# Kernel tuning notes

Hardware: AMD Instinct MI355X
Metric: run time of the kernel (lower is better)

## Reference

```python
import math
import jax, jax.numpy as jnp
import numpy as np

NH, NKV, HD = 16, 8, 128  # n_heads, n_kv_heads, head_dim from config

def setup_inputs() -> dict:
    key = jax.random.key(0)
    ks = jax.random.split(key, 5)
    B, T, D = 2, 2048, 2048
    KV = NKV * HD  # 1024
    s = 1.0 / math.sqrt(D)
    return {
        "x": jax.random.normal(ks[0], (B, T, D), dtype=jnp.float32),
        "Wq": jax.random.normal(ks[1], (D, D), dtype=jnp.float32) * s,
        "Wk": jax.random.normal(ks[2], (KV, D), dtype=jnp.float32) * s,
        "Wv": jax.random.normal(ks[3], (KV, D), dtype=jnp.float32) * s,
        "Wo": jax.random.normal(ks[4], (D, D), dtype=jnp.float32) * s,
    }

def reference(x, Wq, Wk, Wv, Wo):
    B, T, D = x.shape
    groups = NH // NKV
    scale = 1.0 / math.sqrt(HD)
    # Projections (torch Linear: y = x @ W.T)
    q = (x @ Wq.T).reshape(B, T, NH, HD).transpose(0, 2, 1, 3)    # [B, nh, T, hd]
    k = (x @ Wk.T).reshape(B, T, NKV, HD).transpose(0, 2, 1, 3)   # [B, nkv, T, hd]
    v = (x @ Wv.T).reshape(B, T, NKV, HD).transpose(0, 2, 1, 3)   # [B, nkv, T, hd]
    kv_state = jnp.concatenate([k, v], axis=-1)                    # [B, nkv, T, 2*hd]
    # GQA: replicate kv heads (repeat_interleave along head dim)
    k = jnp.repeat(k, groups, axis=1)                              # [B, nh, T, hd]
    v = jnp.repeat(v, groups, axis=1)
    scores = jnp.einsum('bhqd,bhkd->bhqk', q, k) * scale           # [B, nh, T, T]
    causal = jnp.tril(jnp.ones((T, T), dtype=bool))
    scores = jnp.where(causal, scores, jnp.finfo(scores.dtype).min)
    probs = jax.nn.softmax(scores, axis=-1)
    attn = jnp.einsum('bhqk,bhkd->bhqd', probs, v)                 # [B, nh, T, hd]
    attn = attn.transpose(0, 2, 1, 3).reshape(B, T, NH * HD)
    output = attn @ Wo.T
    return (output, kv_state)
```

## Files before the change

### kernel.cpp

```cpp
#include <hip/hip_runtime.h>
#include <hip/hip_bf16.h>
#include <cstdint>
#include <cstddef>

#define DEV __device__ __forceinline__

typedef __attribute__((ext_vector_type(8))) short short8;
typedef __attribute__((ext_vector_type(4))) float f32x4;
typedef __attribute__((ext_vector_type(8))) __bf16 bf16x8;

DEV unsigned short f2bf(float f) {
    unsigned u = __builtin_bit_cast(unsigned, f);
    u += 0x7fffu + ((u >> 16) & 1u);
    return (unsigned short)(u >> 16);
}

DEV unsigned short f2bf_hw(float f) {
    return __builtin_bit_cast(unsigned short, (__bf16)f);
}

DEV f32x4 mfma16(short8 a, short8 b, f32x4 c) {
    return __builtin_amdgcn_mfma_f32_16x16x32_bf16(
        __builtin_bit_cast(bf16x8, a), __builtin_bit_cast(bf16x8, b), c, 0, 0, 0);
}

#define GLD_TO_LDS16(g, l)                                                  \
    __builtin_amdgcn_global_load_lds(                                       \
        (const __attribute__((address_space(1))) void*)(g),                 \
        (__attribute__((address_space(3))) void*)(l), 16, 0, 0)

__global__ void cvt_all(const float* __restrict__ x,  const float* __restrict__ wq,
                        const float* __restrict__ wk, const float* __restrict__ wv,
                        const float* __restrict__ wo,
                        unsigned short* __restrict__ xb,  unsigned short* __restrict__ wqb,
                        unsigned short* __restrict__ wkb, unsigned short* __restrict__ wvb,
                        unsigned short* __restrict__ wob) {
    constexpr int NX = 1048576, NQ = 524288, NK = 262144, NV = 262144, NO = 524288;
    constexpr int C1 = NX, C2 = C1 + NQ, C3 = C2 + NK, C4 = C3 + NV, C5 = C4 + NO;
    int i = blockIdx.x * blockDim.x + threadIdx.x;
    int stride = gridDim.x * blockDim.x;
    for (; i < C5; i += stride) {
        const float* s;
        unsigned short* d;
        int j;
        if (i < C1)      { s = x;  d = xb;  j = i; }
        else if (i < C2) { s = wq; d = wqb; j = i - C1; }
        else if (i < C3) { s = wk; d = wkb; j = i - C2; }
        else if (i < C4) { s = wv; d = wvb; j = i - C3; }
        else             { s = wo; d = wob; j = i - C4; }
        const f32x4* sp = (const f32x4*)(s + (size_t)j * 8);
        f32x4 a = sp[0], bq = sp[1];
        short8 o;
        o[0] = (short)f2bf(a[0]);  o[1] = (short)f2bf(a[1]);
        o[2] = (short)f2bf(a[2]);  o[3] = (short)f2bf(a[3]);
        o[4] = (short)f2bf(bq[0]); o[5] = (short)f2bf(bq[1]);
        o[6] = (short)f2bf(bq[2]); o[7] = (short)f2bf(bq[3]);
        *(short8*)(d + (size_t)j * 8) = o;
    }
}

__global__ __launch_bounds__(256) void transpose_v(
    const unsigned short* __restrict__ src, unsigned short* __restrict__ dst) {
    __shared__ __align__(16) unsigned short tile[64 * 64];
    const int t0 = blockIdx.x * 64;
    const int d0 = blockIdx.y * 64;
    const int b  = blockIdx.z;
    const int tid = threadIdx.x;
#pragma unroll
    for (int p = 0; p < 2; ++p) {
        int ch = tid + p * 256;
        int it = ch >> 3, ic8 = ch & 7;
        short8 v = *(const short8*)(src + (size_t)(b * 2048 + t0 + it) * 1024 + d0 + ic8 * 8);
        *(short8*)&tile[it * 64 + ((ic8 ^ (it & 7)) << 3)] = v;
    }
    __syncthreads();
#pragma unroll
    for (int p = 0; p < 2; ++p) {
        int ch = tid + p * 256;
        int od = ch >> 3, ot8 = ch & 7;
        short8 v;
#pragma unroll
        for (int j = 0; j < 8; ++j) {
            int t = ot8 * 8 + j;
            v[j] = (short)tile[t * 64 + ((((od >> 3) ^ (t & 7)) << 3) | (od & 7))];
        }
        *(short8*)(dst + (size_t)(b * 1024 + d0 + od) * 2048 + t0 + ot8 * 8) = v;
    }
}

__global__ __launch_bounds__(512, 2) void gemm_qkv_8p(
    const unsigned short* __restrict__ A,
    const unsigned short* __restrict__ Wq, const unsigned short* __restrict__ Wk,
    const unsigned short* __restrict__ Wv,
    unsigned short* __restrict__ Qo, unsigned short* __restrict__ Ko,
    unsigned short* __restrict__ Vo, float* __restrict__ kvf) {
    constexpr int K = 2048, BM = 256, KT = K / 64;
    __shared__ __align__(16) unsigned short sA[2][2][BM][32];
    __shared__ __align__(16) unsigned short sB[2][2][BM][32];

    const int tid = threadIdx.x, lane = tid & 63, w = tid >> 6;
    const int wm = w >> 2, wn = w & 3;
    const int lrow = lane & 15, lg = lane >> 4;
    const int m0 = blockIdx.y * BM, n0 = blockIdx.x * BM;

    const unsigned short* Bp;
    unsigned short* Co;
    int c0, ostr, doff = 0;
    bool iskv = false;
    if (n0 < 2048)      { Bp = Wq + (size_t)n0 * K;        Co = Qo; c0 = n0;        ostr = 2048; }
    else if (n0 < 3072) { Bp = Wk + (size_t)(n0-2048) * K; Co = Ko; c0 = n0 - 2048; ostr = 1024; iskv = true; }
    else                { Bp = Wv + (size_t)(n0-3072) * K; Co = Vo; c0 = n0 - 3072; ostr = 1024; iskv = true; doff = 128; }

    const unsigned short* Ab = A + (size_t)m0 * K;

    auto stage = [&](const unsigned short* gcol, unsigned short* lds) {
#pragma unroll
        for (int p = 0; p < 2; ++p) {
            int ch = tid + p * 512;
            int row = ch >> 2;
            int slot = (ch & 3) ^ (row & 3);
            GLD_TO_LDS16(gcol + (size_t)row * K + slot * 8, lds + ch * 8);
        }
    };

    f32x4 acc[8][4];
#pragma unroll
    for (int i = 0; i < 8; ++i)
#pragma unroll
        for (int j = 0; j < 4; ++j) acc[i][j] = (f32x4)0.f;

    const int xoff = (lg * 8) ^ ((lrow & 3) << 3);
    const int arow0 = wm * 128 + lrow;
    const int brow0 = wn * 64 + lrow;

    stage(Ab,      &sA[0][0][0][0]);
    stage(Bp,      &sB[0][0][0][0]);
    stage(Ab + 32, &sA[0][1][0][0]);
    stage(Bp + 32, &sB[0][1][0][0]);
    asm volatile("s_waitcnt vmcnt(4)\n\ts_barrier" ::: "memory");

    for (int kt = 0; kt < KT; ++kt) {
        const int buf = kt & 1, nb = buf ^ 1;
        const bool pre = (kt + 1 < KT);
        const unsigned short* An = Ab + (kt + 1) * 64;
        const unsigned short* Bn = Bp + (kt + 1) * 64;
        short8 bfrag[4], afrag[4];

        if (pre) stage(An, &sA[nb][0][0][0]);
#pragma unroll
        for (int ni = 0; ni < 4; ++ni)
            bfrag[ni] = *(const short8*)(&sB[buf][0][brow0 + ni * 16][0] + xoff);
#pragma unroll
        for (int mi = 0; mi < 4; ++mi)
            afrag[mi] = *(const short8*)(&sA[buf][0][arow0 + mi * 16][0] + xoff);
        __builtin_amdgcn_s_setprio(1);
#pragma unroll
        for (int mi = 0; mi < 4; ++mi)
#pragma unroll
            for (int ni = 0; ni < 4; ++ni)
                acc[mi][ni] = mfma16(afrag[mi], bfrag[ni], acc[mi][ni]);
        __builtin_amdgcn_s_setprio(0);

        if (pre) stage(Bn, &sB[nb][0][0][0]);
#pragma unroll
        for (int mi = 0; mi < 4; ++mi)
            afrag[mi] = *(const short8*)(&sA[buf][0][arow0 + 64 + mi * 16][0] + xoff);
        __builtin_amdgcn_s_setprio(1);
#pragma unroll
        for (int mi = 0; mi < 4; ++mi)
#pragma unroll
            for (int ni = 0; ni < 4; ++ni)
                acc[4 + mi][ni] = mfma16(afrag[mi], bfrag[ni], acc[4 + mi][ni]);
        __builtin_amdgcn_s_setprio(0);

        if (pre) asm volatile("s_waitcnt vmcnt(4)\n\ts_barrier" ::: "memory");
        else     asm volatile("s_waitcnt vmcnt(0)\n\ts_barrier" ::: "memory");

        if (pre) stage(An + 32, &sA[nb][1][0][0]);
#pragma unroll
        for (int ni = 0; ni < 4; ++ni)
            bfrag[ni] = *(const short8*)(&sB[buf][1][brow0 + ni * 16][0] + xoff);
#pragma unroll
        for (int mi = 0; mi < 4; ++mi)
            afrag[mi] = *(const short8*)(&sA[buf][1][arow0 + mi * 16][0] + xoff);
        __builtin_amdgcn_s_setprio(1);
#pragma unroll
        for (int mi = 0; mi < 4; ++mi)
#pragma unroll
            for (int ni = 0; ni < 4; ++ni)
                acc[mi][ni] = mfma16(afrag[mi], bfrag[ni], acc[mi][ni]);
        __builtin_amdgcn_s_setprio(0);

        if (pre) stage(Bn + 32, &sB[nb][1][0][0]);
#pragma unroll
        for (int mi = 0; mi < 4; ++mi)
            afrag[mi] = *(const short8*)(&sA[buf][1][arow0 + 64 + mi * 16][0] + xoff);
        __builtin_amdgcn_s_setprio(1);
#pragma unroll
        for (int mi = 0; mi < 4; ++mi)
#pragma unroll
            for (int ni = 0; ni < 4; ++ni)
                acc[4 + mi][ni] = mfma16(afrag[mi], bfrag[ni], acc[4 + mi][ni]);
        __builtin_amdgcn_s_setprio(0);

        if (pre) asm volatile("s_waitcnt vmcnt(4)\n\ts_barrier" ::: "memory");
    }

    const int lrow4 = (lane >> 4) * 4, lcol = lane & 15;
#pragma unroll
    for (int mi = 0; mi < 8; ++mi) {
#pragma unroll
        for (int ni = 0; ni < 4; ++ni) {
#pragma unroll
            for (int r = 0; r < 4; ++r) {
                int row = m0 + wm * 128 + mi * 16 + lrow4 + r;
                int col = c0 + wn * 64 + ni * 16 + lcol;
                float v = acc[mi][ni][r];
                Co[(size_t)row * ostr + col] = f2bf(v);
                if (iskv) {
                    int b = row >> 11, t = row & 2047;
                    int kh = col >> 7, d = col & 127;
                    kvf[((size_t)(b * 8 + kh) * 2048 + t) * 256 + doff + d] = v;
                }
            }
        }
    }
}

__global__ __launch_bounds__(512, 2) void gemm_o_2p(
    const unsigned short* __restrict__ A, const unsigned short* __restrict__ Bm,
    float* __restrict__ Cf) {
    constexpr int K = 2048, N = 2048, KT = K / 64;
    __shared__ __align__(16) unsigned short sA[2][2][256][32];
    __shared__ __align__(16) unsigned short sB[2][2][128][32];

    const int tid = threadIdx.x, lane = tid & 63, w = tid >> 6;
    const int wm = w >> 1, wn = w & 1;
    const int lrow = lane & 15, lg = lane >> 4;
    const int m0 = blockIdx.y * 256, n0 = blockIdx.x * 128;

    const unsigned short* Ab = A + (size_t)m0 * K;
    const unsigned short* Bb = Bm + (size_t)n0 * K;

    auto stageA = [&](const unsigned short* gcol, unsigned short* lds) {
#pragma unroll
        for (int p = 0; p < 2; ++p) {
            int ch = tid + p * 512;
            int row = ch >> 2;
            int slot = (ch & 3) ^ (row & 3);
            GLD_TO_LDS16(gcol + (size_t)row * K + slot * 8, lds + ch * 8);
        }
    };
    auto stageB = [&](const unsigned short* gcol, unsigned short* lds) {
        int ch = tid;
        int row = ch >> 2;
        int slot = (ch & 3) ^ (row & 3);
        GLD_TO_LDS16(gcol + (size_t)row * K + slot * 8, lds + ch * 8);
    };

    f32x4 acc[4][4];
#pragma unroll
    for (int i = 0; i < 4; ++i)
#pragma unroll
        for (int j = 0; j < 4; ++j) acc[i][j] = (f32x4)0.f;

    const int xoff = (lg * 8) ^ ((lrow & 3) << 3);
    const int arow0 = wm * 64 + lrow;
    const int brow0 = wn * 64 + lrow;

    stageA(Ab,      &sA[0][0][0][0]);
    stageB(Bb,      &sB[0][0][0][0]);
    stageA(Ab + 32, &sA[0][1][0][0]);
    stageB(Bb + 32, &sB[0][1][0][0]);
    asm volatile("s_waitcnt vmcnt(3)\n\ts_barrier" ::: "memory");

    for (int kt = 0; kt < KT; ++kt) {
        const int buf = kt & 1, nb = buf ^ 1;
        const bool pre = (kt + 1 < KT);
        const unsigned short* An = Ab + (kt + 1) * 64;
        const unsigned short* Bn = Bb + (kt + 1) * 64;
        short8 afrag[4], bfrag[4];

        if (pre) { stageA(An, &sA[nb][0][0][0]); stageB(Bn, &sB[nb][0][0][0]); }
#pragma unroll
        for (int ni = 0; ni < 4; ++ni)
            bfrag[ni] = *(const short8*)(&sB[buf][0][brow0 + ni * 16][0] + xoff);
#pragma unroll
        for (int mi = 0; mi < 4; ++mi)
            afrag[mi] = *(const short8*)(&sA[buf][0][arow0 + mi * 16][0] + xoff);
        __builtin_amdgcn_s_setprio(1);
#pragma unroll
        for (int mi = 0; mi < 4; ++mi)
#pragma unroll
            for (int ni = 0; ni < 4; ++ni)
                acc[mi][ni] = mfma16(afrag[mi], bfrag[ni], acc[mi][ni]);
        __builtin_amdgcn_s_setprio(0);

        if (pre) asm volatile("s_waitcnt vmcnt(3)\n\ts_barrier" ::: "memory");
        else     asm volatile("s_waitcnt vmcnt(0)\n\ts_barrier" ::: "memory");

        if (pre) { stageA(An + 32, &sA[nb][1][0][0]); stageB(Bn + 32, &sB[nb][1][0][0]); }
#pragma unroll
        for (int ni = 0; ni < 4; ++ni)
            bfrag[ni] = *(const short8*)(&sB[buf][1][brow0 + ni * 16][0] + xoff);
#pragma unroll
        for (int mi = 0; mi < 4; ++mi)
            afrag[mi] = *(const short8*)(&sA[buf][1][arow0 + mi * 16][0] + xoff);
        __builtin_amdgcn_s_setprio(1);
#pragma unroll
        for (int mi = 0; mi < 4; ++mi)
#pragma unroll
            for (int ni = 0; ni < 4; ++ni)
                acc[mi][ni] = mfma16(afrag[mi], bfrag[ni], acc[mi][ni]);
        __builtin_amdgcn_s_setprio(0);

        if (pre) asm volatile("s_waitcnt vmcnt(3)\n\ts_barrier" ::: "memory");
    }

    const int lrow4 = (lane >> 4) * 4, lcol = lane & 15;
#pragma unroll
    for (int mi = 0; mi < 4; ++mi)
#pragma unroll
        for (int ni = 0; ni < 4; ++ni)
#pragma unroll
            for (int r = 0; r < 4; ++r) {
                int row = m0 + wm * 64 + mi * 16 + lrow4 + r;
                int col = n0 + wn * 64 + ni * 16 + lcol;
                Cf[(size_t)row * N + col] = acc[mi][ni][r];
            }
}

__global__ __launch_bounds__(512, 2) void attn_fwd(
    const unsigned short* __restrict__ Qb, const unsigned short* __restrict__ Kb,
    const unsigned short* __restrict__ Vtg, unsigned short* __restrict__ Ob) {
    constexpr int T = 2048, DQ = 2048, DKV = 1024, HD = 128;
    constexpr float SC2 = 0.08838834764831845f * 1.4426950408889634f;
    constexpr float SHIFT = 8.0f * 1.4426950408889634f;
    __shared__ __align__(16) unsigned short Ks[2][64][128];
    __shared__ __align__(16) unsigned short Vs[2][128][64];
    __shared__ __align__(16) unsigned short Ps[8][16][64];

    const int bx = blockIdx.x, kh = blockIdx.y, b = blockIdx.z;
    const int qtile = b ? (31 - bx) : bx;
    const int tid = threadIdx.x, lane = tid & 63, w = tid >> 6;
    const int h = kh * 2 + (w >> 2);
    const int lrow = lane & 15, lg = lane >> 4;
    const int qt0 = qtile * 64;
    const int qrow0 = qt0 + (w & 3) * 16;
    const size_t bT = (size_t)b * T;

    short8 qf[4];
    {
        const unsigned short* qbase = Qb + (bT + qrow0 + lrow) * DQ + h * HD + lg * 8;
#pragma unroll
        for (int kc = 0; kc < 4; ++kc) qf[kc] = *(const short8*)(qbase + kc * 32);
    }

    int kr[2], kc8[2], vd[2], vk8[2];
#pragma unroll
    for (int p = 0; p < 2; ++p) {
        int ch = tid + p * 512;
        kr[p] = ch >> 4;  kc8[p] = ch & 15;
        vd[p] = ch >> 3;  vk8[p] = ch & 7;
    }
    const unsigned short* kbase = Kb + bT * DKV + kh * HD;
    const unsigned short* vbase = Vtg + (size_t)(b * 8 + kh) * 128 * T;
    short8 kreg[2], vreg[2];
    auto gload = [&](int kt) {
#pragma unroll
        for (int p = 0; p < 2; ++p) {
            kreg[p] = *(const short8*)(kbase + (size_t)(kt * 64 + kr[p]) * DKV + kc8[p] * 8);
            vreg[p] = *(const short8*)(vbase + (size_t)vd[p] * T + kt * 64 + vk8[p] * 8);
        }
    };
    auto lwrite = [&](int buf) {
#pragma unroll
        for (int p = 0; p < 2; ++p) {
            *(short8*)&Ks[buf][kr[p]][(kc8[p] ^ (kr[p] & 15)) << 3] = kreg[p];
            *(short8*)&Vs[buf][vd[p]][(vk8[p] ^ (vd[p] & 7)) << 3] = vreg[p];
        }
    };

    f32x4 o[8];
#pragma unroll
    for (int i = 0; i < 8; ++i) o[i] = (f32x4)0.f;
    float rsum[4] = {0.f, 0.f, 0.f, 0.f};

    const int nkt = qtile + 1;
    gload(0);
    for (int kt = 0; kt < nkt; ++kt) {
        const int kt0 = kt * 64;
        const int buf = kt & 1;
        lwrite(buf);
        __syncthreads();
        if (kt + 1 < nkt) gload(kt + 1);

        f32x4 s[4];
        __builtin_amdgcn_s_setprio(1);
#pragma unroll
        for (int nt = 0; nt < 4; ++nt) {
            s[nt] = (f32x4)0.f;
#pragma unroll
            for (int kc = 0; kc < 4; ++kc) {
                short8 kf = *(const short8*)&Ks[buf][nt * 16 + lrow][((kc * 4 + lg) ^ lrow) << 3];
                s[nt] = mfma16(qf[kc], kf, s[nt]);
            }
        }
        __builtin_amdgcn_s_setprio(0);

        const int qabs = qrow0 + lg * 4;
        const bool diag = (kt == qtile);
#pragma unroll
        for (int nt = 0; nt < 4; ++nt) {
            int kcol = kt0 + nt * 16 + lrow;
#pragma unroll
            for (int r = 0; r < 4; ++r) {
                float p = exp2f(fmaf(s[nt][r], SC2, -SHIFT));
                if (diag && kcol > qabs + r) p = 0.f;
                rsum[r] += p;
                int q = lg * 4 + r;
                Ps[w][q][((((nt * 2) + (lrow >> 3)) ^ (q & 7)) << 3) | (lrow & 7)] = f2bf_hw(p);
            }
        }

        __builtin_amdgcn_s_setprio(1);
#pragma unroll
        for (int kc2 = 0; kc2 < 2; ++kc2) {
            short8 pf = *(const short8*)&Ps[w][lrow][((kc2 * 4 + lg) ^ (lrow & 7)) << 3];
#pragma unroll
            for (int dt = 0; dt < 8; ++dt) {
                int d = dt * 16 + lrow;
                short8 vf = *(const short8*)&Vs[buf][d][((kc2 * 4 + lg) ^ (d & 7)) << 3];
                o[dt] = mfma16(pf, vf, o[dt]);
            }
        }
        __builtin_amdgcn_s_setprio(0);
    }

#pragma unroll
    for (int r = 0; r < 4; ++r) {
        float v = rsum[r];
        v += __shfl_xor(v, 1);
        v += __shfl_xor(v, 2);
        v += __shfl_xor(v, 4);
        v += __shfl_xor(v, 8);
        float inv = 1.f / v;
        int row = qrow0 + lg * 4 + r;
        unsigned short* obase = Ob + (bT + row) * DQ + h * HD + lrow;
#pragma unroll
        for (int dt = 0; dt < 8; ++dt) obase[dt * 16] = f2bf_hw(o[dt][r] * inv);
    }
}

extern "C" void kernel_launch(void* const* d_in, const int* in_sizes, int n_in,
                              void* d_out, int out_size, void* d_ws, size_t ws_size,
                              hipStream_t stream) {
    (void)in_sizes; (void)n_in; (void)out_size; (void)ws_size;
    const float* x  = (const float*)d_in[0];
    const float* Wq = (const float*)d_in[1];
    const float* Wk = (const float*)d_in[2];
    const float* Wv = (const float*)d_in[3];
    const float* Wo = (const float*)d_in[4];
    float* out = (float*)d_out;
    float* kv_out = out + (size_t)8388608;

    unsigned short* xb   = (unsigned short*)d_ws;
    unsigned short* wqb  = xb   + 8388608;
    unsigned short* wkb  = wqb  + 4194304;
    unsigned short* wvb  = wkb  + 2097152;
    unsigned short* wob  = wvb  + 2097152;
    unsigned short* qb   = wob  + 4194304;
    unsigned short* kb   = qb   + 8388608;
    unsigned short* vt   = kb   + 4194304;
    unsigned short* ab   = vt   + 4194304;
    unsigned short* vtmp = ab;

    cvt_all<<<dim3(2048), dim3(256), 0, stream>>>(x, Wq, Wk, Wv, Wo,
                                                  xb, wqb, wkb, wvb, wob);
    gemm_qkv_8p<<<dim3(16, 16), 512, 0, stream>>>(xb, wqb, wkb, wvb, qb, kb, vtmp, kv_out);
    transpose_v<<<dim3(32, 16, 2), 256, 0, stream>>>(vtmp, vt);
    attn_fwd<<<dim3(32, 8, 2), 512, 0, stream>>>(qb, kb, vt, ab);
    gemm_o_2p<<<dim3(16, 16), 512, 0, stream>>>(ab, wob, out);
}
```

Before: 252.1 us.

## Stream K/V directly to LDS and pass P through register permutes

```diff
diff --git a/kernel.cpp b/kernel.cpp
--- a/kernel.cpp
+++ b/kernel.cpp
@@ -7,6 +7,7 @@
 
 typedef __attribute__((ext_vector_type(8))) short short8;
 typedef __attribute__((ext_vector_type(4))) float f32x4;
+typedef __attribute__((ext_vector_type(4))) unsigned int uint4v;
 typedef __attribute__((ext_vector_type(8))) __bf16 bf16x8;
 
 DEV unsigned short f2bf(float f) {
@@ -330,7 +331,7 @@
             }
 }
 
-__global__ __launch_bounds__(512, 2) void attn_fwd(
+__global__ __launch_bounds__(512, 4) void attn_fwd(
     const unsigned short* __restrict__ Qb, const unsigned short* __restrict__ Kb,
     const unsigned short* __restrict__ Vtg, unsigned short* __restrict__ Ob) {
     constexpr int T = 2048, DQ = 2048, DKV = 1024, HD = 128;
@@ -338,7 +339,6 @@
     constexpr float SHIFT = 8.0f * 1.4426950408889634f;
     __shared__ __align__(16) unsigned short Ks[2][64][128];
     __shared__ __align__(16) unsigned short Vs[2][128][64];
-    __shared__ __align__(16) unsigned short Ps[8][16][64];
 
     const int bx = blockIdx.x, kh = blockIdx.y, b = blockIdx.z;
     const int qtile = b ? (31 - bx) : bx;
@@ -356,44 +356,42 @@
         for (int kc = 0; kc < 4; ++kc) qf[kc] = *(const short8*)(qbase + kc * 32);
     }
 
-    int kr[2], kc8[2], vd[2], vk8[2];
-#pragma unroll
-    for (int p = 0; p < 2; ++p) {
-        int ch = tid + p * 512;
-        kr[p] = ch >> 4;  kc8[p] = ch & 15;
-        vd[p] = ch >> 3;  vk8[p] = ch & 7;
-    }
     const unsigned short* kbase = Kb + bT * DKV + kh * HD;
     const unsigned short* vbase = Vtg + (size_t)(b * 8 + kh) * 128 * T;
-    short8 kreg[2], vreg[2];
-    auto gload = [&](int kt) {
+
+    auto stage = [&](int kt, int buf) {
 #pragma unroll
         for (int p = 0; p < 2; ++p) {
-            kreg[p] = *(const short8*)(kbase + (size_t)(kt * 64 + kr[p]) * DKV + kc8[p] * 8);
-            vreg[p] = *(const short8*)(vbase + (size_t)vd[p] * T + kt * 64 + vk8[p] * 8);
+            int ch = (p * 8 + w) * 64 + lane;
+            int kr = ch >> 4, g = (ch & 15) ^ (kr & 15);
+            GLD_TO_LDS16(kbase + (size_t)(kt * 64 + kr) * DKV + g * 8,
+                         &Ks[buf][0][0] + ch * 8);
+        }
+#pragma unroll
+        for (int p = 0; p < 2; ++p) {
+            int ch = (p * 8 + w) * 64 + lane;
+            int d = ch >> 3, g = (ch & 7) ^ (d & 7);
+            GLD_TO_LDS16(vbase + (size_t)d * T + kt * 64 + g * 8,
+                         &Vs[buf][0][0] + ch * 8);
         }
     };
-    auto lwrite = [&](int buf) {
-#pragma unroll
-        for (int p = 0; p < 2; ++p) {
-            *(short8*)&Ks[buf][kr[p]][(kc8[p] ^ (kr[p] & 15)) << 3] = kreg[p];
-            *(short8*)&Vs[buf][vd[p]][(vk8[p] ^ (vd[p] & 7)) << 3] = vreg[p];
-        }
-    };
 
     f32x4 o[8];
 #pragma unroll
     for (int i = 0; i < 8; ++i) o[i] = (f32x4)0.f;
-    float rsum[4] = {0.f, 0.f, 0.f, 0.f};
+    float rsum = 0.f;
+
+    const int l1b = ((((lg & 1) << 5) + lrow) << 2);
+    const int l2b = l1b + 64;
+    const bool sh = (lg & 2) != 0;
+    const int qabs = qrow0 + lrow;
 
     const int nkt = qtile + 1;
-    gload(0);
+    stage(0, 0);
+    __syncthreads();
     for (int kt = 0; kt < nkt; ++kt) {
-        const int kt0 = kt * 64;
         const int buf = kt & 1;
-        lwrite(buf);
-        __syncthreads();
-        if (kt + 1 < nkt) gload(kt + 1);
+        if (kt + 1 < nkt) stage(kt + 1, buf ^ 1);
 
         f32x4 s[4];
         __builtin_amdgcn_s_setprio(1);
@@ -403,48 +401,69 @@
 #pragma unroll
             for (int kc = 0; kc < 4; ++kc) {
                 short8 kf = *(const short8*)&Ks[buf][nt * 16 + lrow][((kc * 4 + lg) ^ lrow) << 3];
-                s[nt] = mfma16(qf[kc], kf, s[nt]);
+                s[nt] = mfma16(kf, qf[kc], s[nt]);
             }
         }
         __builtin_amdgcn_s_setprio(0);
 
-        const int qabs = qrow0 + lg * 4;
         const bool diag = (kt == qtile);
+        const int k00 = kt * 64 + lg * 4;
+        unsigned dwA[4], dwB[4];
 #pragma unroll
         for (int nt = 0; nt < 4; ++nt) {
-            int kcol = kt0 + nt * 16 + lrow;
-#pragma unroll
-            for (int r = 0; r < 4; ++r) {
-                float p = exp2f(fmaf(s[nt][r], SC2, -SHIFT));
-                if (diag && kcol > qabs + r) p = 0.f;
-                rsum[r] += p;
-                int q = lg * 4 + r;
-                Ps[w][q][((((nt * 2) + (lrow >> 3)) ^ (q & 7)) << 3) | (lrow & 7)] = f2bf_hw(p);
+            int k0 = k00 + nt * 16;
+            float p0 = exp2f(fmaf(s[nt][0], SC2, -SHIFT));
+            float p1 = exp2f(fmaf(s[nt][1], SC2, -SHIFT));
+            float p2 = exp2f(fmaf(s[nt][2], SC2, -SHIFT));
+            float p3 = exp2f(fmaf(s[nt][3], SC2, -SHIFT));
+            if (diag) {
+                p0 = (k0 + 0 > qabs) ? 0.f : p0;
+                p1 = (k0 + 1 > qabs) ? 0.f : p1;
+                p2 = (k0 + 2 > qabs) ? 0.f : p2;
+                p3 = (k0 + 3 > qabs) ? 0.f : p3;
             }
-        }
-
-        __builtin_amdgcn_s_setprio(1);
+            rsum += (p0 + p1) + (p2 + p3);
+            dwA[nt] = (unsigned)f2bf_hw(p0) | ((unsigned)f2bf_hw(p1) << 16);
+            dwB[nt] = (unsigned)f2bf_hw(p2) | ((unsigned)f2bf_hw(p3) << 16);
+        }
+
 #pragma unroll
         for (int kc2 = 0; kc2 < 2; ++kc2) {
-            short8 pf = *(const short8*)&Ps[w][lrow][((kc2 * 4 + lg) ^ (lrow & 7)) << 3];
+            unsigned aL = dwA[2 * kc2], aH = dwA[2 * kc2 + 1];
+            unsigned bL = dwB[2 * kc2], bH = dwB[2 * kc2 + 1];
+            unsigned r0l = (unsigned)__builtin_amdgcn_ds_bpermute(l1b, (int)aL);
+            unsigned r0h = (unsigned)__builtin_amdgcn_ds_bpermute(l1b, (int)aH);
+            unsigned r1l = (unsigned)__builtin_amdgcn_ds_bpermute(l1b, (int)bL);
+            unsigned r1h = (unsigned)__builtin_amdgcn_ds_bpermute(l1b, (int)bH);
+            unsigned r2l = (unsigned)__builtin_amdgcn_ds_bpermute(l2b, (int)aL);
+            unsigned r2h = (unsigned)__builtin_amdgcn_ds_bpermute(l2b, (int)aH);
+            unsigned r3l = (unsigned)__builtin_amdgcn_ds_bpermute(l2b, (int)bL);
+            unsigned r3h = (unsigned)__builtin_amdgcn_ds_bpermute(l2b, (int)bH);
+            uint4v pw;
+            pw[0] = sh ? r0h : r0l;
+            pw[1] = sh ? r1h : r1l;
+            pw[2] = sh ? r2h : r2l;
+            pw[3] = sh ? r3h : r3l;
+            short8 pf = __builtin_bit_cast(short8, pw);
+            __builtin_amdgcn_s_setprio(1);
 #pragma unroll
             for (int dt = 0; dt < 8; ++dt) {
-                int d = dt * 16 + lrow;
-                short8 vf = *(const short8*)&Vs[buf][d][((kc2 * 4 + lg) ^ (d & 7)) << 3];
+                short8 vf = *(const short8*)&Vs[buf][dt * 16 + lrow][((kc2 * 4 + lg) ^ (lrow & 7)) << 3];
                 o[dt] = mfma16(pf, vf, o[dt]);
             }
-        }
-        __builtin_amdgcn_s_setprio(0);
-    }
-
+            __builtin_amdgcn_s_setprio(0);
+        }
+
+        if (kt + 1 < nkt) __syncthreads();
+    }
+
+    float tot = rsum;
+    tot += __shfl_xor(tot, 16);
+    tot += __shfl_xor(tot, 32);
 #pragma unroll
     for (int r = 0; r < 4; ++r) {
-        float v = rsum[r];
-        v += __shfl_xor(v, 1);
-        v += __shfl_xor(v, 2);
-        v += __shfl_xor(v, 4);
-        v += __shfl_xor(v, 8);
-        float inv = 1.f / v;
+        float rt = __shfl(tot, lg * 4 + r);
+        float inv = 1.f / rt;
         int row = qrow0 + lg * 4 + r;
         unsigned short* obase = Ob + (bT + row) * DQ + h * HD + lrow;
 #pragma unroll
```

Result: faster. 233.3 us (-7.5%).
